# Kernel optimization log

Hardware: AMD Instinct MI355X
Metric: run time of the kernel (lower is better)

The kernel has to match this reference:

```python
import jax, jax.numpy as jnp
import numpy as np

B, S, D, H = 2, 2048, 512, 8


def setup_inputs() -> dict:
    key = jax.random.key(0)
    ks = jax.random.split(key, 9)
    scale = 1.0 / np.sqrt(D)
    x = jax.random.normal(ks[0], (B, S, D), dtype=jnp.float32)
    # Per-head full-width projections, stacked over heads: [H, D, D]
    Wq = jax.random.normal(ks[1], (H, D, D), dtype=jnp.float32) * scale
    Wk = jax.random.normal(ks[2], (H, D, D), dtype=jnp.float32) * scale
    Wv = jax.random.normal(ks[3], (H, D, D), dtype=jnp.float32) * scale
    bq = jax.random.normal(ks[4], (H, D), dtype=jnp.float32) * 0.01
    bk = jax.random.normal(ks[5], (H, D), dtype=jnp.float32) * 0.01
    bv = jax.random.normal(ks[6], (H, D), dtype=jnp.float32) * 0.01
    Wo = jax.random.normal(ks[7], (H * D, D), dtype=jnp.float32) * (1.0 / np.sqrt(H * D))
    bo = jax.random.normal(ks[8], (D,), dtype=jnp.float32) * 0.01
    return {"x": x, "Wq": Wq, "bq": bq, "Wk": Wk, "bk": bk, "Wv": Wv, "bv": bv, "Wo": Wo, "bo": bo}


def reference(x, Wq, bq, Wk, bk, Wv, bv, Wo, bo):
    # Batched per-head projections: [B,S,D] x [H,D,E] -> [B,H,S,E]
    q = jnp.einsum('bsd,hde->bhse', x, Wq) + bq[None, :, None, :]
    k = jnp.einsum('bsd,hde->bhse', x, Wk) + bk[None, :, None, :]
    v = jnp.einsum('bsd,hde->bhse', x, Wv) + bv[None, :, None, :]
    # NOTE: original module has NO 1/sqrt(d) scaling
    scores = jnp.einsum('bhse,bhte->bhst', q, k)  # [B,H,S,S]
    attn = jax.nn.softmax(scores, axis=-1)
    out = jnp.einsum('bhst,bhte->bhse', attn, v)  # [B,H,S,D]
    # Concat heads along feature dim: [B,S,H*D]
    cat = out.transpose(0, 2, 1, 3).reshape(B, S, H * D)
    return cat @ Wo + bo
```

## Files before the change

### kernel.cpp

```cpp
#include <hip/hip_runtime.h>

typedef _Float16 f16;
typedef _Float16 f16x8 __attribute__((ext_vector_type(8)));
typedef float f32x4 __attribute__((ext_vector_type(4)));

#define B_ 2
#define S_ 2048
#define D_ 512
#define H_ 8

__device__ inline void async_ld16(const void* g, void* l) {
  __builtin_amdgcn_global_load_lds((__attribute__((address_space(1))) void*)(g),
                                   (__attribute__((address_space(3))) void*)(l),
                                   16, 0, 0);
}

__global__ __launch_bounds__(256) void cvt_f16(const float* __restrict__ src,
                                               f16* __restrict__ dst, long n) {
  long i = (long)blockIdx.x * 256 + threadIdx.x;
  if (i >= n) return;
  dst[i] = (f16)src[i];
}

__global__ __launch_bounds__(256) void transpose_f32(const float* __restrict__ src,
                                                     f16* __restrict__ dst, int R, int C) {
  __shared__ float t[32][33];
  size_t zoff = (size_t)blockIdx.z * R * C;
  const float* s = src + zoff;
  int tx = threadIdx.x;
  int ty = threadIdx.y;
  int c0 = blockIdx.x * 32, r0 = blockIdx.y * 32;
#pragma unroll
  for (int i = 0; i < 4; ++i)
    t[ty + i * 8][tx] = s[(size_t)(r0 + ty + i * 8) * C + c0 + tx];
  __syncthreads();
#pragma unroll
  for (int i = 0; i < 4; ++i)
    dst[zoff + (size_t)(c0 + ty + i * 8) * R + r0 + tx] = (f16)t[tx][ty + i * 8];
}

__global__ __launch_bounds__(256) void reduce_out(const float* __restrict__ part,
                                                  const float* __restrict__ bo,
                                                  float* __restrict__ out, long n, int nslab) {
  long i = (long)blockIdx.x * 256 + threadIdx.x;
  if (i >= n) return;
  float v = bo[i & (D_ - 1)];
  for (int s = 0; s < nslab; ++s) v += part[(long)s * n + i];
  out[i] = v;
}

struct GemmArgs {
  const f16 *A, *Bm;
  void* C;
  const float* bias;
  float* Mloc;
  int K, lda, ldb, ldc;
  int zbase, NG, PBG;
  long sAp, sAb, sAg, sAz;
  long sBp, sBb, sBg, sBz;
  long sCp, sCb, sCg, sCz;
  long sbp, sbb, sbg, sbz;
  long sMlz;
};

template <typename OutT, int BIAS, bool PEXP>
__global__ __launch_bounds__(256) void gemm_nt(GemmArgs p) {
  int zloc = blockIdx.z;
  int zi = p.zbase + zloc;
  int pp = zi / p.PBG; int rz = zi - pp * p.PBG;
  int bb = rz / p.NG;  int g = rz - bb * p.NG;
  const f16* A  = p.A + (pp * p.sAp + bb * p.sAb + g * p.sAg + (long)zloc * p.sAz);
  const f16* Bm = p.Bm + (pp * p.sBp + bb * p.sBb + g * p.sBg + (long)zloc * p.sBz);
  OutT* C = (OutT*)p.C + (pp * p.sCp + bb * p.sCb + g * p.sCg + (long)zloc * p.sCz);
  const float* bias = nullptr;
  if (BIAS) bias = p.bias + (pp * p.sbp + bb * p.sbb + g * p.sbg + (long)zloc * p.sbz);

  __shared__ f16 lA[4096];
  __shared__ f16 lB[4096];
  __shared__ float lMx[PEXP ? 256 : 1];

  int tid = threadIdx.x;
  int lane = tid & 63;
  int w = tid >> 6;
  int wm = (w >> 1) << 6;
  int wn = (w & 1) << 6;
  long bm = (long)blockIdx.y * 128;
  long bn = (long)blockIdx.x * 128;

  f32x4 acc[4][4] = {};
  int qd = lane >> 4;
  int fr = lane & 15;

  int q0 = tid, q1 = tid + 256;
  int r0s = q0 >> 2, c0s = (q0 & 3) ^ ((r0s >> 1) & 3);
  int r1s = q1 >> 2, c1s = (q1 & 3) ^ ((r1s >> 1) & 3);

  for (int k0 = 0; k0 < p.K; k0 += 32) {
    long oa0 = (bm + r0s) * (long)p.lda + (k0 + c0s * 8);
    long oa1 = (bm + r1s) * (long)p.lda + (k0 + c1s * 8);
    long ob0 = (bn + r0s) * (long)p.ldb + (k0 + c0s * 8);
    long ob1 = (bn + r1s) * (long)p.ldb + (k0 + c1s * 8);
    __syncthreads();
    async_ld16(A + oa0,  lA + (size_t)q0 * 8);
    async_ld16(A + oa1,  lA + (size_t)q1 * 8);
    async_ld16(Bm + ob0, lB + (size_t)q0 * 8);
    async_ld16(Bm + ob1, lB + (size_t)q1 * 8);
    __syncthreads();

    f16x8 ah[4], bh[4];
#pragma unroll
    for (int i = 0; i < 4; ++i) {
      int m = wm + i * 16 + fr;
      ah[i] = *(const f16x8*)(lA + ((size_t)m * 4 + (qd ^ ((m >> 1) & 3))) * 8);
      int n = wn + i * 16 + fr;
      bh[i] = *(const f16x8*)(lB + ((size_t)n * 4 + (qd ^ ((n >> 1) & 3))) * 8);
    }
#pragma unroll
    for (int i = 0; i < 4; ++i)
#pragma unroll
      for (int j = 0; j < 4; ++j)
        acc[i][j] = __builtin_amdgcn_mfma_f32_16x16x32_f16(ah[i], bh[j], acc[i][j], 0, 0, 0);
  }

  int rr0 = qd * 4;
  if (PEXP) {
#pragma unroll
    for (int i = 0; i < 4; ++i) {
#pragma unroll
      for (int r = 0; r < 4; ++r) {
        float v = fmaxf(fmaxf(acc[i][0][r], acc[i][1][r]),
                        fmaxf(acc[i][2][r], acc[i][3][r]));
        v = fmaxf(v, __shfl_xor(v, 1, 64));
        v = fmaxf(v, __shfl_xor(v, 2, 64));
        v = fmaxf(v, __shfl_xor(v, 4, 64));
        v = fmaxf(v, __shfl_xor(v, 8, 64));
        if (fr == 0) lMx[(w & 1) * 128 + wm + i * 16 + rr0 + r] = v;
      }
    }
    __syncthreads();
    if (tid < 128) {
      float ml = fmaxf(lMx[tid], lMx[128 + tid]);
      p.Mloc[(long)zloc * p.sMlz + (long)blockIdx.x * S_ + bm + tid] = ml;
    }
#pragma unroll
    for (int i = 0; i < 4; ++i) {
#pragma unroll
      for (int r = 0; r < 4; ++r) {
        int rl = wm + i * 16 + rr0 + r;
        float ml = fmaxf(lMx[rl], lMx[128 + rl]);
        long row = bm + rl;
#pragma unroll
        for (int j = 0; j < 4; ++j) {
          long col = bn + wn + j * 16 + fr;
          ((f16*)C)[row * (long)p.ldc + col] = (f16)__expf(acc[i][j][r] - ml);
        }
      }
    }
  } else {
#pragma unroll
    for (int i = 0; i < 4; ++i) {
#pragma unroll
      for (int j = 0; j < 4; ++j) {
#pragma unroll
        for (int r = 0; r < 4; ++r) {
          long row = bm + wm + i * 16 + rr0 + r;
          long col = bn + wn + j * 16 + fr;
          float v = acc[i][j][r];
          if (BIAS == 1) v += bias[col];
          if (BIAS == 2) v += bias[row];
          C[row * (long)p.ldc + col] = (OutT)v;
        }
      }
    }
  }
}

struct QkvArgs {
  const f16 *xh, *wqk, *wv;
  f16 *qk, *vT;
  const float *bqk, *bv;
};

template <int MH, int NH>
__device__ inline void phase_mfma(const f16* L, int cur, int qr, int qc,
                                  int qd, int fr, f32x4 (&acc)[2][2][4][2]) {
  const f16* Ab = L + cur * 32768 + MH * 8192;
  const f16* Bb = L + cur * 32768 + 16384 + NH * 8192;
  f16x8 af[4][2], bf[2][2];
#pragma unroll
  for (int i = 0; i < 4; ++i) {
    int rr = qr * 64 + i * 16 + fr;
#pragma unroll
    for (int ks = 0; ks < 2; ++ks) {
      int cc = ks * 4 + qd;
      af[i][ks] = *(const f16x8*)(Ab + ((size_t)rr * 8 + (cc ^ ((rr >> 1) & 7))) * 8);
    }
  }
#pragma unroll
  for (int j = 0; j < 2; ++j) {
    int rr = qc * 32 + j * 16 + fr;
#pragma unroll
    for (int ks = 0; ks < 2; ++ks) {
      int cc = ks * 4 + qd;
      bf[j][ks] = *(const f16x8*)(Bb + ((size_t)rr * 8 + (cc ^ ((rr >> 1) & 7))) * 8);
    }
  }
  __builtin_amdgcn_s_setprio(1);
#pragma unroll
  for (int i = 0; i < 4; ++i)
#pragma unroll
    for (int j = 0; j < 2; ++j)
#pragma unroll
      for (int ks = 0; ks < 2; ++ks)
        acc[MH][NH][i][j] = __builtin_amdgcn_mfma_f32_16x16x32_f16(
            af[i][ks], bf[j][ks], acc[MH][NH][i][j], 0, 0, 0);
  __builtin_amdgcn_s_setprio(0);
}

#define QWAIT(N)                                              \
  asm volatile("s_waitcnt vmcnt(" #N ")" ::: "memory");       \
  __builtin_amdgcn_s_barrier();                               \
  __builtin_amdgcn_sched_barrier(0);
#define QBAR()                                                \
  __builtin_amdgcn_s_barrier();                               \
  __builtin_amdgcn_sched_barrier(0);

__global__ __launch_bounds__(512, 2) void qkv_proj8(QkvArgs p) {
  const long SD = (long)S_ * D_, DD = (long)D_ * D_, DS = (long)D_ * S_;
  int zi = blockIdx.z;
  int pp = zi >> 4;
  int r = zi & 15;
  int b = r >> 3, h = r & 7;
  int bid = blockIdx.x;
  const f16 *A, *Bm;
  f16* C;
  const float* bias;
  long bm, bn;
  int ldc;
  bool biasRow;
  if (pp < 2) {
    A = p.xh + (long)b * SD;
    Bm = p.wqk + ((long)pp * 8 + h) * DD;
    C = p.qk + (long)zi * SD;
    bias = p.bqk + ((long)pp * 8 + h) * D_;
    bm = (long)(bid >> 1) * 256; bn = (long)(bid & 1) * 256;
    ldc = D_; biasRow = false;
  } else {
    A = p.wv + (long)h * DD;
    Bm = p.xh + (long)b * SD;
    C = p.vT + (long)(b * 8 + h) * DS;
    bias = p.bv + (long)h * D_;
    bm = (long)(bid >> 3) * 256; bn = (long)(bid & 7) * 256;
    ldc = S_; biasRow = true;
  }

  __shared__ f16 L[65536];

  int tid = threadIdx.x;
  int lane = tid & 63;
  int w = tid >> 6;
  int qr = w >> 2, qc = w & 3;
  int qd = lane >> 4, fr = lane & 15;

  f32x4 acc[2][2][4][2] = {};

  int srl = w * 16 + (lane >> 3);
  int sslot = lane & 7;

  auto stage = [&](const f16* src, long row0, int kb, int ldsBase) {
#pragma unroll
    for (int k = 0; k < 2; ++k) {
      int rl = srl + k * 8;
      int c = sslot ^ ((rl >> 1) & 7);
      async_ld16(src + (row0 + rl) * (long)D_ + (kb + c * 8),
                 L + ldsBase + (w * 2 + k) * 512 + lane * 8);
    }
  };
  auto iA = [&](int buf, int hh, int t) {
    stage(A, bm + hh * 128, t * 64, buf * 32768 + hh * 8192);
  };
  auto iB = [&](int buf, int hh, int t) {
    stage(Bm, bn + hh * 128, t * 64, buf * 32768 + 16384 + hh * 8192);
  };

  iA(0, 0, 0); iB(0, 0, 0); iB(0, 1, 0); iA(0, 1, 0);

  int cur = 0;
  for (int t = 0; t < 7; ++t) {
    int nxt = cur ^ 1;
    iA(nxt, 0, t + 1);
    QWAIT(6)
    phase_mfma<0, 0>(L, cur, qr, qc, qd, fr, acc);
    iB(nxt, 0, t + 1);
    QWAIT(6)
    phase_mfma<0, 1>(L, cur, qr, qc, qd, fr, acc);
    iB(nxt, 1, t + 1);
    QWAIT(6)
    phase_mfma<1, 0>(L, cur, qr, qc, qd, fr, acc);
    iA(nxt, 1, t + 1);
    QBAR()
    phase_mfma<1, 1>(L, cur, qr, qc, qd, fr, acc);
    cur = nxt;
  }
  QWAIT(4)
  phase_mfma<0, 0>(L, cur, qr, qc, qd, fr, acc);
  QWAIT(2)
  phase_mfma<0, 1>(L, cur, qr, qc, qd, fr, acc);
  QWAIT(0)
  phase_mfma<1, 0>(L, cur, qr, qc, qd, fr, acc);
  QBAR()
  phase_mfma<1, 1>(L, cur, qr, qc, qd, fr, acc);

  int rr0 = qd * 4;
#pragma unroll
  for (int mh = 0; mh < 2; ++mh)
#pragma unroll
    for (int nh = 0; nh < 2; ++nh)
#pragma unroll
      for (int i = 0; i < 4; ++i)
#pragma unroll
        for (int j = 0; j < 2; ++j)
#pragma unroll
          for (int rl = 0; rl < 4; ++rl) {
            long row = bm + mh * 128 + qr * 64 + i * 16 + rr0 + rl;
            long col = bn + nh * 128 + qc * 32 + j * 16 + fr;
            float v = acc[mh][nh][i][j][rl] + (biasRow ? bias[row] : bias[col]);
            C[row * (long)ldc + col] = (f16)v;
          }
}

struct Sc8Args {
  const f16 *Q, *K;
  f16* P;
  float* Ml;
};

__global__ __launch_bounds__(512, 2) void scores8(Sc8Args p) {
  int zloc = blockIdx.z;
  const f16* A  = p.Q + (long)zloc * S_ * D_;
  const f16* Bm = p.K + (long)zloc * S_ * D_;
  f16* C = p.P + (long)zloc * (long)S_ * S_;
  float* Ml = p.Ml + (long)zloc * 16L * S_;
  int bid = blockIdx.x;
  long bm = (long)(bid >> 3) * 256, bn = (long)(bid & 7) * 256;

  __shared__ f16 L[65536];
  __shared__ float lMx2[4][256];

  int tid = threadIdx.x;
  int lane = tid & 63;
  int w = tid >> 6;
  int qr = w >> 2, qc = w & 3;
  int qd = lane >> 4, fr = lane & 15;

  f32x4 acc[2][2][4][2] = {};

  int srl = w * 16 + (lane >> 3);
  int sslot = lane & 7;

  auto stage = [&](const f16* src, long row0, int kb, int ldsBase) {
#pragma unroll
    for (int k = 0; k < 2; ++k) {
      int rl = srl + k * 8;
      int c = sslot ^ ((rl >> 1) & 7);
      async_ld16(src + (row0 + rl) * (long)D_ + (kb + c * 8),
                 L + ldsBase + (w * 2 + k) * 512 + lane * 8);
    }
  };
  auto iA = [&](int buf, int hh, int t) {
    stage(A, bm + hh * 128, t * 64, buf * 32768 + hh * 8192);
  };
  auto iB = [&](int buf, int hh, int t) {
    stage(Bm, bn + hh * 128, t * 64, buf * 32768 + 16384 + hh * 8192);
  };

  iA(0, 0, 0); iB(0, 0, 0); iB(0, 1, 0); iA(0, 1, 0);

  int cur = 0;
  for (int t = 0; t < 7; ++t) {
    int nxt = cur ^ 1;
    iA(nxt, 0, t + 1);
    QWAIT(6)
    phase_mfma<0, 0>(L, cur, qr, qc, qd, fr, acc);
    iB(nxt, 0, t + 1);
    QWAIT(6)
    phase_mfma<0, 1>(L, cur, qr, qc, qd, fr, acc);
    iB(nxt, 1, t + 1);
    QWAIT(6)
    phase_mfma<1, 0>(L, cur, qr, qc, qd, fr, acc);
    iA(nxt, 1, t + 1);
    QBAR()
    phase_mfma<1, 1>(L, cur, qr, qc, qd, fr, acc);
    cur = nxt;
  }
  QWAIT(4)
  phase_mfma<0, 0>(L, cur, qr, qc, qd, fr, acc);
  QWAIT(2)
  phase_mfma<0, 1>(L, cur, qr, qc, qd, fr, acc);
  QWAIT(0)
  phase_mfma<1, 0>(L, cur, qr, qc, qd, fr, acc);
  QBAR()
  phase_mfma<1, 1>(L, cur, qr, qc, qd, fr, acc);

#pragma unroll
  for (int mh = 0; mh < 2; ++mh)
#pragma unroll
    for (int i = 0; i < 4; ++i)
#pragma unroll
      for (int rl = 0; rl < 4; ++rl) {
        float v = fmaxf(fmaxf(acc[mh][0][i][0][rl], acc[mh][0][i][1][rl]),
                        fmaxf(acc[mh][1][i][0][rl], acc[mh][1][i][1][rl]));
        v = fmaxf(v, __shfl_xor(v, 1, 64));
        v = fmaxf(v, __shfl_xor(v, 2, 64));
        v = fmaxf(v, __shfl_xor(v, 4, 64));
        v = fmaxf(v, __shfl_xor(v, 8, 64));
        if (fr == 0) lMx2[qc][mh * 128 + qr * 64 + i * 16 + qd * 4 + rl] = v;
      }
  __syncthreads();
  if (tid < 256) {
    float ml = fmaxf(fmaxf(lMx2[0][tid], lMx2[1][tid]),
                     fmaxf(lMx2[2][tid], lMx2[3][tid]));
    int cb0 = (bid & 7) * 2;
    Ml[(long)cb0 * S_ + bm + tid] = ml;
    Ml[(long)(cb0 + 1) * S_ + bm + tid] = ml;
  }
#pragma unroll
  for (int mh = 0; mh < 2; ++mh)
#pragma unroll
    for (int i = 0; i < 4; ++i)
#pragma unroll
      for (int rl = 0; rl < 4; ++rl) {
        int rowLoc = mh * 128 + qr * 64 + i * 16 + qd * 4 + rl;
        float ml = fmaxf(fmaxf(lMx2[0][rowLoc], lMx2[1][rowLoc]),
                         fmaxf(lMx2[2][rowLoc], lMx2[3][rowLoc]));
        long row = bm + rowLoc;
#pragma unroll
        for (int nh = 0; nh < 2; ++nh)
#pragma unroll
          for (int j = 0; j < 2; ++j) {
            long col = bn + nh * 128 + qc * 32 + j * 16 + fr;
            C[row * (long)S_ + col] = (f16)__expf(acc[mh][nh][i][j][rl] - ml);
          }
      }
}

struct PvArgs {
  const f16* S; const float* Ml; const f16* V; f16* C;
  int ldc, zbase, NG;
  long sVz, sCb, sCg;
};
__global__ __launch_bounds__(256) void pv_flash(PvArgs p) {
  int zloc = blockIdx.z;
  int zi = p.zbase + zloc;
  int bb = zi / p.NG; int g = zi - bb * p.NG;
  const f16* Sm = p.S + (long)zloc * S_ * S_;
  const float* Ml = p.Ml + (long)zloc * 16 * S_;
  const f16* V = p.V + (long)zloc * p.sVz;
  f16* C = p.C + bb * p.sCb + g * p.sCg;

  __shared__ f16 lP[2][64 * 32];
  __shared__ f16 lV[2][128 * 32];

  int tid = threadIdx.x;
  int lane = tid & 63;
  int w = tid >> 6;
  long bm = (long)blockIdx.y * 64;
  long bn = (long)blockIdx.x * 128;
  int e0 = (w & 1) << 6;
  int m0 = (w >> 1) << 5;

  int qd = lane >> 4;
  int fr = lane & 15;

  f32x4 acc[2][4] = {};
  f32x4 lacc[2] = {};
  f16x8 ones;
#pragma unroll
  for (int j = 0; j < 8; ++j) ones[j] = (f16)1.0f;

  float mg[2];
#pragma unroll
  for (int i = 0; i < 2; ++i) {
    float m = -1e30f;
#pragma unroll
    for (int cb = 0; cb < 16; ++cb)
      m = fmaxf(m, Ml[cb * S_ + bm + m0 + i * 16 + fr]);
    mg[i] = m;
  }
  f16 al16[2];

  int rs = tid >> 2, cs = (tid & 3) ^ ((rs >> 1) & 3);

  for (int k0 = 0; k0 < S_; k0 += 64) {
    if ((k0 & 127) == 0) {
      int cb = k0 >> 7;
#pragma unroll
      for (int i = 0; i < 2; ++i)
        al16[i] = (f16)__expf(Ml[cb * S_ + bm + m0 + i * 16 + fr] - mg[i]);
    }
    __syncthreads();
#pragma unroll
    for (int t = 0; t < 2; ++t) {
      async_ld16(Sm + (bm + rs) * (long)S_ + (k0 + t * 32 + cs * 8),
                 lP[t] + (size_t)tid * 8);
#pragma unroll
      for (int j = 0; j < 2; ++j) {
        int q = j * 256 + tid;
        int rv = q >> 2, cv = (q & 3) ^ ((rv >> 1) & 3);
        async_ld16(V + (bn + rv) * (long)S_ + (k0 + t * 32 + cv * 8),
                   lV[t] + (size_t)q * 8);
      }
    }
    __syncthreads();

#pragma unroll
    for (int t = 0; t < 2; ++t) {
      f16x8 ah[2], bh[4];
#pragma unroll
      for (int i = 0; i < 2; ++i) {
        int m = m0 + i * 16 + fr;
        ah[i] = *(const f16x8*)(lP[t] + ((size_t)m * 4 + (qd ^ ((m >> 1) & 3))) * 8);
#pragma unroll
        for (int j = 0; j < 8; ++j) ah[i][j] *= al16[i];
      }
#pragma unroll
      for (int j = 0; j < 4; ++j) {
        int n = e0 + j * 16 + fr;
        bh[j] = *(const f16x8*)(lV[t] + ((size_t)n * 4 + (qd ^ ((n >> 1) & 3))) * 8);
      }
#pragma unroll
      for (int i = 0; i < 2; ++i) {
        lacc[i] = __builtin_amdgcn_mfma_f32_16x16x32_f16(ah[i], ones, lacc[i], 0, 0, 0);
#pragma unroll
        for (int j = 0; j < 4; ++j)
          acc[i][j] = __builtin_amdgcn_mfma_f32_16x16x32_f16(ah[i], bh[j], acc[i][j], 0, 0, 0);
      }
    }
  }

  int rr0 = qd * 4;
#pragma unroll
  for (int i = 0; i < 2; ++i) {
    float inv[4];
#pragma unroll
    for (int r = 0; r < 4; ++r) inv[r] = 1.0f / lacc[i][r];
#pragma unroll
    for (int j = 0; j < 4; ++j) {
#pragma unroll
      for (int r = 0; r < 4; ++r) {
        long row = bm + m0 + i * 16 + rr0 + r;
        long col = bn + e0 + j * 16 + fr;
        C[row * (long)p.ldc + col] = (f16)(acc[i][j][r] * inv[r]);
      }
    }
  }
}

extern "C" void kernel_launch(void* const* d_in, const int* in_sizes, int n_in,
                              void* d_out, int out_size, void* d_ws, size_t ws_size,
                              hipStream_t stream) {
  const float* x  = (const float*)d_in[0];
  const float* Wq = (const float*)d_in[1];
  const float* bq = (const float*)d_in[2];
  const float* Wk = (const float*)d_in[3];
  const float* bk = (const float*)d_in[4];
  const float* Wv = (const float*)d_in[5];
  const float* bv = (const float*)d_in[6];
  const float* Wo = (const float*)d_in[7];
  const float* bo = (const float*)d_in[8];
  float* out = (float*)d_out;

  auto al = [](size_t v) { return (v + 255) & ~(size_t)255; };
  const size_t eX = (size_t)B_ * S_ * D_;
  const size_t eW = (size_t)H_ * D_ * D_;
  const size_t eSS = (size_t)S_ * S_;
  const long SD = (long)S_ * D_;
  const long DD = (long)D_ * D_;
  const long DS = (long)D_ * S_;

  size_t fixed = al(eX * 2) + al(2 * eW * 2) + al(eW * 2) + al(eW * 2)
               + al(2ULL * H_ * D_ * 4);
  int NB = 1, GH = 1, GS = 1; bool found = false;
  for (int nb = 2; nb >= 1 && !found; --nb)
    for (int gh = 8; gh >= 1 && !found; gh >>= 1)
      for (int gs = nb * gh; gs >= 1 && !found; gs >>= 1) {
        size_t need = fixed + al((size_t)nb * S_ * H_ * D_ * 2)
                    + al(2ULL * nb * gh * S_ * D_ * 2)
                    + al((size_t)nb * gh * D_ * S_ * 2)
                    + al(4ULL * nb * SD * 4)
                    + al((size_t)gs * eSS * 2)
                    + al((size_t)gs * 16 * S_ * 4);
        if (need <= ws_size) { NB = nb; GH = gh; GS = gs; found = true; }
      }

  char* p0 = (char*)d_ws;
  size_t off = 0;
  f16* xh    = (f16*)(p0 + off); off += al(eX * 2);
  f16* wqk   = (f16*)(p0 + off); off += al(2 * eW * 2);
  f16* wv    = (f16*)(p0 + off); off += al(eW * 2);
  f16* wo    = (f16*)(p0 + off); off += al(eW * 2);
  float* bqk = (float*)(p0 + off); off += al(2ULL * H_ * D_ * 4);
  f16* catb  = (f16*)(p0 + off); off += al((size_t)NB * S_ * H_ * D_ * 2);
  f16* qk    = (f16*)(p0 + off); off += al(2ULL * NB * GH * S_ * D_ * 2);
  f16* vT    = (f16*)(p0 + off); off += al((size_t)NB * GH * D_ * S_ * 2);
  float* opart = (float*)(p0 + off); off += al(4ULL * NB * SD * 4);
  f16* scores = (f16*)(p0 + off); off += al((size_t)GS * eSS * 2);
  float* mloc = (float*)(p0 + off);

  cvt_f16<<<dim3((unsigned)((eX + 255) / 256)), 256, 0, stream>>>(x, xh, (long)eX);
  dim3 tb(32, 8, 1);
  transpose_f32<<<dim3(16, 16, H_), tb, 0, stream>>>(Wq, wqk, D_, D_);
  transpose_f32<<<dim3(16, 16, H_), tb, 0, stream>>>(Wk, wqk + eW, D_, D_);
  transpose_f32<<<dim3(16, 16, H_), tb, 0, stream>>>(Wv, wv, D_, D_);
  transpose_f32<<<dim3(16, 128, 1), tb, 0, stream>>>(Wo, wo, H_ * D_, D_);
  hipMemcpyAsync(bqk, bq, (size_t)H_ * D_ * 4, hipMemcpyDeviceToDevice, stream);
  hipMemcpyAsync(bqk + H_ * D_, bk, (size_t)H_ * D_ * 4, hipMemcpyDeviceToDevice, stream);

  for (int b0 = 0; b0 < B_; b0 += NB) {
    for (int h0 = 0; h0 < H_; h0 += GH) {
      if (NB == 2 && GH == 8) {
        QkvArgs a{xh, wqk, wv, qk, vT, bqk, bv};
        qkv_proj8<<<dim3(16, 1, 48), 512, 0, stream>>>(a);
      } else {
        {
          GemmArgs a{};
          a.A = xh + (long)b0 * SD;
          a.Bm = wqk + (long)h0 * DD;
          a.C = qk; a.bias = bqk + (long)h0 * D_;
          a.K = D_; a.lda = D_; a.ldb = D_; a.ldc = D_;
          a.zbase = 0; a.NG = GH; a.PBG = NB * GH;
          a.sAb = SD;
          a.sBp = (long)H_ * DD; a.sBg = DD;
          a.sCz = SD;
          a.sbp = (long)H_ * D_; a.sbg = D_;
          gemm_nt<f16, 1, false><<<dim3(4, 16, 2 * NB * GH), 256, 0, stream>>>(a);
        }
        {
          GemmArgs a{};
          a.A = wv + (long)h0 * DD; a.Bm = xh + (long)b0 * SD;
          a.C = vT; a.bias = bv + (long)h0 * D_;
          a.K = D_; a.lda = D_; a.ldb = D_; a.ldc = S_;
          a.zbase = 0; a.NG = GH; a.PBG = NB * GH;
          a.sAg = DD;
          a.sBb = SD;
          a.sCz = DS;
          a.sbg = D_;
          gemm_nt<f16, 2, false><<<dim3(16, 4, NB * GH), 256, 0, stream>>>(a);
        }
      }
      for (int g0 = 0; g0 < NB * GH; g0 += GS) {
        {
          Sc8Args a{qk + (long)g0 * SD, qk + ((long)NB * GH + g0) * SD,
                    scores, mloc};
          scores8<<<dim3(64, 1, GS), 512, 0, stream>>>(a);
        }
        {
          PvArgs a{};
          a.S = scores; a.Ml = mloc; a.V = vT + (long)g0 * DS;
          a.C = catb + (long)h0 * D_;
          a.ldc = H_ * D_; a.zbase = g0; a.NG = GH;
          a.sVz = DS; a.sCb = (long)S_ * H_ * D_; a.sCg = D_;
          pv_flash<<<dim3(4, S_ / 64, GS), 256, 0, stream>>>(a);
        }
      }
    }
    {
      GemmArgs a{};
      a.A = catb; a.Bm = wo;
      a.C = opart;
      a.K = 1024; a.lda = H_ * D_; a.ldb = H_ * D_; a.ldc = D_;
      a.zbase = 0; a.NG = 4; a.PBG = NB * 4;
      a.sAb = (long)S_ * H_ * D_; a.sAg = 1024;
      a.sBg = 1024;
      a.sCb = SD; a.sCg = (long)NB * SD;
      gemm_nt<float, 0, false><<<dim3(4, 16, NB * 4), 256, 0, stream>>>(a);
    }
    reduce_out<<<dim3((unsigned)(((long)NB * SD + 255) / 256)), 256, 0, stream>>>(
        opart, bo, out + (long)b0 * SD, (long)NB * SD, 4);
  }
}
```

Before: 458.3 us.

## Rewrite PV kernel with 256x128 tiles, 8 waves, and pipelined LDS double buffering

Replaces the 64x128-tile, 4-wave PV kernel with a 512-thread kernel where each block computes a 256x128 output tile. Score and V tiles are double-buffered in LDS with staggered async loads and explicit vmcnt waits, and the per-row max values are staged once into LDS. The row-sum MFMA is halved by pre-adding the two k-slices in fp16, and s_setprio raises priority around the MFMA bursts. The larger tile cuts redundant loads of V and scores but uses far more LDS, which may limit occupancy, and the fp16 pre-add slightly changes the precision of the row sums.

```diff
diff --git a/kernel.cpp b/kernel.cpp
--- a/kernel.cpp
+++ b/kernel.cpp
@@ -449,111 +449,176 @@
   int ldc, zbase, NG;
   long sVz, sCb, sCg;
 };
-__global__ __launch_bounds__(256) void pv_flash(PvArgs p) {
+
+template <int MH>
+__device__ inline void pv_phase(const f16* L, int cur, int qr, int qc, int qd,
+                                int fr, const f16 (&al)[2][4],
+                                f32x4 (&acc)[2][4][2], f32x4 (&lacc)[2][4],
+                                f16x8 ones) {
+  const f16* Ab = L + cur * 24576 + MH * 8192;
+  const f16* Bb = L + cur * 24576 + 16384;
+  f16x8 af[4][2], bf[2][2];
+#pragma unroll
+  for (int i = 0; i < 4; ++i) {
+    int rr = qr * 64 + i * 16 + fr;
+#pragma unroll
+    for (int ks = 0; ks < 2; ++ks) {
+      int cc = ks * 4 + qd;
+      af[i][ks] = *(const f16x8*)(Ab + ((size_t)rr * 8 + (cc ^ ((rr >> 1) & 7))) * 8);
+#pragma unroll
+      for (int e = 0; e < 8; ++e) af[i][ks][e] *= al[MH][i];
+    }
+  }
+#pragma unroll
+  for (int j = 0; j < 2; ++j) {
+    int rr = qc * 32 + j * 16 + fr;
+#pragma unroll
+    for (int ks = 0; ks < 2; ++ks) {
+      int cc = ks * 4 + qd;
+      bf[j][ks] = *(const f16x8*)(Bb + ((size_t)rr * 8 + (cc ^ ((rr >> 1) & 7))) * 8);
+    }
+  }
+  __builtin_amdgcn_s_setprio(1);
+#pragma unroll
+  for (int i = 0; i < 4; ++i) {
+    f16x8 a2 = af[i][0] + af[i][1];
+    lacc[MH][i] = __builtin_amdgcn_mfma_f32_16x16x32_f16(a2, ones, lacc[MH][i], 0, 0, 0);
+#pragma unroll
+    for (int j = 0; j < 2; ++j)
+#pragma unroll
+      for (int ks = 0; ks < 2; ++ks)
+        acc[MH][i][j] = __builtin_amdgcn_mfma_f32_16x16x32_f16(
+            af[i][ks], bf[j][ks], acc[MH][i][j], 0, 0, 0);
+  }
+  __builtin_amdgcn_s_setprio(0);
+}
+
+__global__ __launch_bounds__(512, 2) void pv_flash8(PvArgs p) {
   int zloc = blockIdx.z;
   int zi = p.zbase + zloc;
   int bb = zi / p.NG; int g = zi - bb * p.NG;
   const f16* Sm = p.S + (long)zloc * S_ * S_;
-  const float* Ml = p.Ml + (long)zloc * 16 * S_;
+  const float* MlG = p.Ml + (long)zloc * 16 * S_;
   const f16* V = p.V + (long)zloc * p.sVz;
   f16* C = p.C + bb * p.sCb + g * p.sCg;
 
-  __shared__ f16 lP[2][64 * 32];
-  __shared__ f16 lV[2][128 * 32];
+  __shared__ f16 L[49152];
+  __shared__ float lMl[4096];
 
   int tid = threadIdx.x;
   int lane = tid & 63;
   int w = tid >> 6;
-  long bm = (long)blockIdx.y * 64;
-  long bn = (long)blockIdx.x * 128;
-  int e0 = (w & 1) << 6;
-  int m0 = (w >> 1) << 5;
-
-  int qd = lane >> 4;
-  int fr = lane & 15;
-
-  f32x4 acc[2][4] = {};
-  f32x4 lacc[2] = {};
+  int qr = w >> 2, qc = w & 3;
+  int qd = lane >> 4, fr = lane & 15;
+
+  int bid = blockIdx.x;
+  long bm = (long)(bid >> 2) * 256;
+  long bn = (long)(bid & 3) * 128;
+
+  f32x4 acc[2][4][2] = {};
+  f32x4 lacc[2][4] = {};
   f16x8 ones;
 #pragma unroll
-  for (int j = 0; j < 8; ++j) ones[j] = (f16)1.0f;
-
-  float mg[2];
-#pragma unroll
-  for (int i = 0; i < 2; ++i) {
-    float m = -1e30f;
-#pragma unroll
-    for (int cb = 0; cb < 16; ++cb)
-      m = fmaxf(m, Ml[cb * S_ + bm + m0 + i * 16 + fr]);
-    mg[i] = m;
-  }
-  f16 al16[2];
-
-  int rs = tid >> 2, cs = (tid & 3) ^ ((rs >> 1) & 3);
-
-  for (int k0 = 0; k0 < S_; k0 += 64) {
-    if ((k0 & 127) == 0) {
-      int cb = k0 >> 7;
-#pragma unroll
-      for (int i = 0; i < 2; ++i)
-        al16[i] = (f16)__expf(Ml[cb * S_ + bm + m0 + i * 16 + fr] - mg[i]);
-    }
-    __syncthreads();
-#pragma unroll
-    for (int t = 0; t < 2; ++t) {
-      async_ld16(Sm + (bm + rs) * (long)S_ + (k0 + t * 32 + cs * 8),
-                 lP[t] + (size_t)tid * 8);
-#pragma unroll
-      for (int j = 0; j < 2; ++j) {
-        int q = j * 256 + tid;
-        int rv = q >> 2, cv = (q & 3) ^ ((rv >> 1) & 3);
-        async_ld16(V + (bn + rv) * (long)S_ + (k0 + t * 32 + cv * 8),
-                   lV[t] + (size_t)q * 8);
-      }
-    }
-    __syncthreads();
-
-#pragma unroll
-    for (int t = 0; t < 2; ++t) {
-      f16x8 ah[2], bh[4];
-#pragma unroll
-      for (int i = 0; i < 2; ++i) {
-        int m = m0 + i * 16 + fr;
-        ah[i] = *(const f16x8*)(lP[t] + ((size_t)m * 4 + (qd ^ ((m >> 1) & 3))) * 8);
-#pragma unroll
-        for (int j = 0; j < 8; ++j) ah[i][j] *= al16[i];
-      }
-#pragma unroll
-      for (int j = 0; j < 4; ++j) {
-        int n = e0 + j * 16 + fr;
-        bh[j] = *(const f16x8*)(lV[t] + ((size_t)n * 4 + (qd ^ ((n >> 1) & 3))) * 8);
-      }
-#pragma unroll
-      for (int i = 0; i < 2; ++i) {
-        lacc[i] = __builtin_amdgcn_mfma_f32_16x16x32_f16(ah[i], ones, lacc[i], 0, 0, 0);
-#pragma unroll
-        for (int j = 0; j < 4; ++j)
-          acc[i][j] = __builtin_amdgcn_mfma_f32_16x16x32_f16(ah[i], bh[j], acc[i][j], 0, 0, 0);
-      }
-    }
-  }
+  for (int e = 0; e < 8; ++e) ones[e] = (f16)1.0f;
+
+  int srl = w * 16 + (lane >> 3);
+  int sslot = lane & 7;
+
+  auto stage = [&](const f16* src, long row0, int kb, int ldsBase) {
+#pragma unroll
+    for (int k = 0; k < 2; ++k) {
+      int rl = srl + k * 8;
+      int c = sslot ^ ((rl >> 1) & 7);
+      async_ld16(src + (row0 + rl) * (long)S_ + (kb + c * 8),
+                 L + ldsBase + (w * 2 + k) * 512 + lane * 8);
+    }
+  };
+  auto iA = [&](int buf, int hh, int t) {
+    stage(Sm, bm + hh * 128, t * 64, buf * 24576 + hh * 8192);
+  };
+  auto iB = [&](int buf, int t) {
+    stage(V, bn, t * 64, buf * 24576 + 16384);
+  };
+
+#pragma unroll
+  for (int k = 0; k < 2; ++k) {
+    int cb = k * 8 + w;
+    async_ld16(MlG + (long)cb * S_ + bm + lane * 4,
+               (char*)lMl + (size_t)cb * 1024 + (size_t)lane * 16);
+  }
+  iA(0, 0, 0); iB(0, 0); iA(0, 1, 0);
+  asm volatile("s_waitcnt vmcnt(6)" ::: "memory");
+  __builtin_amdgcn_s_barrier();
+
+  float mg[2][4];
+  f16 al[2][4];
+#pragma unroll
+  for (int mh = 0; mh < 2; ++mh)
+#pragma unroll
+    for (int i = 0; i < 4; ++i) {
+      int rloc = mh * 128 + qr * 64 + i * 16 + fr;
+      float m = -1e30f;
+#pragma unroll
+      for (int cb = 0; cb < 16; ++cb)
+        m = fmaxf(m, lMl[cb * 256 + rloc]);
+      mg[mh][i] = m;
+      al[mh][i] = (f16)__expf(lMl[rloc] - m);
+    }
+
+  int cur = 0;
+  for (int t = 0; t < 31; ++t) {
+    int nxt = cur ^ 1;
+    if (t && (t & 1) == 0) {
+      int cb = t >> 1;
+#pragma unroll
+      for (int mh = 0; mh < 2; ++mh)
+#pragma unroll
+        for (int i = 0; i < 4; ++i) {
+          int rloc = mh * 128 + qr * 64 + i * 16 + fr;
+          al[mh][i] = (f16)__expf(lMl[cb * 256 + rloc] - mg[mh][i]);
+        }
+    }
+    iA(nxt, 0, t + 1);
+    QWAIT(4)
+    pv_phase<0>(L, cur, qr, qc, qd, fr, al, acc, lacc, ones);
+    iB(nxt, t + 1);
+    iA(nxt, 1, t + 1);
+    QWAIT(6)
+    pv_phase<1>(L, cur, qr, qc, qd, fr, al, acc, lacc, ones);
+    cur = nxt;
+  }
+  {
+    int cb = 15;
+#pragma unroll
+    for (int mh = 0; mh < 2; ++mh)
+#pragma unroll
+      for (int i = 0; i < 4; ++i) {
+        int rloc = mh * 128 + qr * 64 + i * 16 + fr;
+        al[mh][i] = (f16)__expf(lMl[cb * 256 + rloc] - mg[mh][i]);
+      }
+  }
+  QWAIT(2)
+  pv_phase<0>(L, cur, qr, qc, qd, fr, al, acc, lacc, ones);
+  QWAIT(0)
+  pv_phase<1>(L, cur, qr, qc, qd, fr, al, acc, lacc, ones);
 
   int rr0 = qd * 4;
 #pragma unroll
-  for (int i = 0; i < 2; ++i) {
-    float inv[4];
-#pragma unroll
-    for (int r = 0; r < 4; ++r) inv[r] = 1.0f / lacc[i][r];
-#pragma unroll
-    for (int j = 0; j < 4; ++j) {
-#pragma unroll
-      for (int r = 0; r < 4; ++r) {
-        long row = bm + m0 + i * 16 + rr0 + r;
-        long col = bn + e0 + j * 16 + fr;
-        C[row * (long)p.ldc + col] = (f16)(acc[i][j][r] * inv[r]);
-      }
-    }
-  }
+  for (int mh = 0; mh < 2; ++mh)
+#pragma unroll
+    for (int i = 0; i < 4; ++i) {
+      float inv[4];
+#pragma unroll
+      for (int rl = 0; rl < 4; ++rl) inv[rl] = 1.0f / lacc[mh][i][rl];
+#pragma unroll
+      for (int j = 0; j < 2; ++j)
+#pragma unroll
+        for (int rl = 0; rl < 4; ++rl) {
+          long row = bm + mh * 128 + qr * 64 + i * 16 + rr0 + rl;
+          long col = bn + qc * 32 + j * 16 + fr;
+          C[row * (long)p.ldc + col] = (f16)(acc[mh][i][j][rl] * inv[rl]);
+        }
+    }
 }
 
 extern "C" void kernel_launch(void* const* d_in, const int* in_sizes, int n_in,
@@ -660,7 +725,7 @@
           a.C = catb + (long)h0 * D_;
           a.ldc = H_ * D_; a.zbase = g0; a.NG = GH;
           a.sVz = DS; a.sCb = (long)S_ * H_ * D_; a.sCg = D_;
-          pv_flash<<<dim3(4, S_ / 64, GS), 256, 0, stream>>>(a);
+          pv_flash8<<<dim3(32, 1, GS), 512, 0, stream>>>(a);
         }
       }
     }
```

Result: no change. 452.2 us, median of 2 (-1.3%).
